# Performance work log

Hardware: AMD Instinct MI355X
Metric: run time of the kernel (lower is better)

The kernel has to match this reference:

```python
import jax, jax.numpy as jnp
import numpy as np

N_HEAD = 16
D_MODEL = 1024
D_K = D_MODEL // N_HEAD  # 64, also d_v
B, S = 8, 1024


def setup_inputs() -> dict:
    key = jax.random.key(0)
    ks = jax.random.split(key, 7)
    sc = 1.0 / np.sqrt(D_MODEL)
    return {
        "q": jax.random.normal(ks[0], (B, S, D_MODEL), jnp.float32),
        "k": jax.random.normal(ks[1], (B, S, D_MODEL), jnp.float32),
        "v": jax.random.normal(ks[2], (B, S, D_MODEL), jnp.float32),
        "Wq": jax.random.normal(ks[3], (N_HEAD, D_MODEL, D_K), jnp.float32) * sc,
        "Wk": jax.random.normal(ks[4], (N_HEAD, D_MODEL, D_K), jnp.float32) * sc,
        "Wv": jax.random.normal(ks[5], (D_MODEL, D_K), jnp.float32) * sc,  # shared across heads
        "Wo": jax.random.normal(ks[6], (D_K, D_MODEL), jnp.float32) * (1.0 / np.sqrt(D_K)),
    }


def reference(q, k, v, Wq, Wk, Wv, Wo):
    # Faithful to original: qs, ks, vs are ALL projected from q (k, v args unused),
    # and Wv is shared across all heads. Dropout is identity (rate 0 / eval).
    qs = jnp.einsum('bsd,hdk->hbsk', q, Wq)          # [H,B,S,dk]
    kk = jnp.einsum('bsd,hdk->hbsk', q, Wk)          # [H,B,S,dk]
    vs = jnp.einsum('bsd,dk->bsk', q, Wv)            # [B,S,dv] shared
    scale = 1.0 / jnp.sqrt(jnp.asarray(D_K, jnp.float32))
    scores = jnp.einsum('hbik,hbjk->hbij', qs, kk) * scale  # [H,B,S,S]
    attn = jax.nn.softmax(scores, axis=-1)
    head = jnp.einsum('hbij,bjk->hbik', attn, vs)    # [H,B,S,dv]
    pooled = jnp.mean(head, axis=0)                  # mean over heads, not concat
    out = jnp.einsum('bsk,kd->bsd', pooled, Wo)      # [B,S,d_model]
    return (out, attn)
```

## Files before the change

kernel.cpp:

```cpp
#include <hip/hip_runtime.h>
#include <hip/hip_bf16.h>
#include <stdint.h>

#define NC 2112

typedef __attribute__((ext_vector_type(8))) short bf16x8;
typedef __attribute__((ext_vector_type(4))) float f32x4;

static __device__ __forceinline__ unsigned short f2bf(float f) {
  uint32_t u = __builtin_bit_cast(uint32_t, f);
  u += 0x7FFFu + ((u >> 16) & 1u);
  return (unsigned short)(u >> 16);
}
static __device__ __forceinline__ float bf2f(unsigned short u) {
  return __builtin_bit_cast(float, ((uint32_t)u) << 16);
}
static __device__ __forceinline__ void gload16(const unsigned short* g, unsigned short* l) {
  __builtin_amdgcn_global_load_lds((const __attribute__((address_space(1))) void*)g,
                                   (__attribute__((address_space(3))) void*)l, 16, 0, 0);
}

__global__ void k_convert_q(const float* __restrict__ q, unsigned short* __restrict__ qbf) {
  int i = blockIdx.x * blockDim.x + threadIdx.x;
  float4 v = ((const float4*)q)[i];
  ushort4 o;
  o.x = f2bf(v.x); o.y = f2bf(v.y); o.z = f2bf(v.z); o.w = f2bf(v.w);
  ((ushort4*)qbf)[i] = o;
}

__global__ void k_build_wcatT(const float* __restrict__ Wq, const float* __restrict__ Wk,
                              const float* __restrict__ Wv, unsigned short* __restrict__ wt) {
  int t = blockIdx.x * blockDim.x + threadIdx.x;
  int c = t >> 7;
  int k0 = (t & 127) << 3;
  unsigned short o[8];
#pragma unroll
  for (int i = 0; i < 8; ++i) {
    int k = k0 + i;
    float v;
    if (c < 1024)      v = Wq[((size_t)(c >> 6) * 1024 + k) * 64 + (c & 63)];
    else if (c < 2048) v = Wk[((size_t)((c - 1024) >> 6) * 1024 + k) * 64 + (c & 63)];
    else               v = Wv[(size_t)k * 64 + (c - 2048)];
    o[i] = f2bf(v);
  }
  *(ushort4*)&wt[(size_t)c * 1024 + k0]     = *(ushort4*)&o[0];
  *(ushort4*)&wt[(size_t)c * 1024 + k0 + 4] = *(ushort4*)&o[4];
}

__global__ __launch_bounds__(256) void k_gemm(const unsigned short* __restrict__ A,
                                              const unsigned short* __restrict__ Bt,
                                              unsigned short* __restrict__ C,
                                              unsigned short* __restrict__ vst) {
  __shared__ unsigned short As[128 * 32];
  __shared__ unsigned short Bs[128 * 32];
  const int L = blockIdx.x;
  const int wi = (L & 7) * 136 + (L >> 3);
  const int tn = wi % 17, tm = wi / 17;
  const int rowBase = tm * 128, colBase = tn * 128;
  const int t = threadIdx.x;
  const int wave = t >> 6, lane = t & 63;
  const int wm = wave >> 1, wn = wave & 1;
  const int l15 = lane & 15, l4 = lane >> 4;
  f32x4 acc[4][4] = {};
  for (int kt = 0; kt < 1024; kt += 32) {
#pragma unroll
    for (int i = 0; i < 2; ++i) {
      int e = (t + i * 256) * 8;
      int r = e >> 5, c = e & 31;
      gload16(&A[(size_t)(rowBase + r) * 1024 + kt + c], &As[e]);
      int rb = colBase + r; rb = rb < NC ? rb : (NC - 1);
      gload16(&Bt[(size_t)rb * 1024 + kt + c], &Bs[e]);
    }
    __syncthreads();
    bf16x8 af[4], bfr[4];
#pragma unroll
    for (int m = 0; m < 4; ++m) af[m] = *(const bf16x8*)&As[(wm * 64 + m * 16 + l15) * 32 + l4 * 8];
#pragma unroll
    for (int n = 0; n < 4; ++n) bfr[n] = *(const bf16x8*)&Bs[(wn * 64 + n * 16 + l15) * 32 + l4 * 8];
#pragma unroll
    for (int m = 0; m < 4; ++m)
#pragma unroll
      for (int n = 0; n < 4; ++n)
        acc[m][n] = __builtin_amdgcn_mfma_f32_16x16x32_bf16(af[m], bfr[n], acc[m][n], 0, 0, 0);
    __syncthreads();
  }
#pragma unroll
  for (int m = 0; m < 4; ++m)
#pragma unroll
    for (int n = 0; n < 4; ++n) {
      int col = colBase + wn * 64 + n * 16 + l15;
      int row0 = rowBase + wm * 64 + m * 16 + l4 * 4;
      if (col < 2048) {
#pragma unroll
        for (int i = 0; i < 4; ++i)
          C[(size_t)(row0 + i) * NC + col] = f2bf(acc[m][n][i]);
      } else if (col < NC) {
        int d = col - 2048;
#pragma unroll
        for (int i = 0; i < 4; ++i) {
          int rg = row0 + i;
          vst[((size_t)(rg >> 10) * 64 + d) * 1024 + (rg & 1023)] = f2bf(acc[m][n][i]);
        }
      }
    }
}

__global__ __launch_bounds__(512, 4) void k_attn(const unsigned short* __restrict__ G,
                                                 const unsigned short* __restrict__ vst,
                                                 float* __restrict__ attn,
                                                 float* __restrict__ head) {
  __shared__ unsigned short SP[32][1032];
  __shared__ float rs[32][8];
  const int L = blockIdx.x;
  const int wi = (L & 7) * 512 + (L >> 3);
  const int qt = wi & 31, b = (wi >> 5) & 7, h = wi >> 8;
  const int t = threadIdx.x, wave = t >> 6, lane = t & 63;
  const int l15 = lane & 15, l4 = lane >> 4;

  const unsigned short* Gb = G + (size_t)b * 1024 * NC;

  bf16x8 qf[2][2];
#pragma unroll
  for (int m = 0; m < 2; ++m)
#pragma unroll
    for (int ks = 0; ks < 2; ++ks)
      qf[m][ks] = *(const bf16x8*)&Gb[(size_t)(qt * 32 + m * 16 + l15) * NC + h * 64 + ks * 32 + l4 * 8];

  const float scale = 0.125f;
  float psum[2][4] = {};
#pragma unroll
  for (int half = 0; half < 2; ++half) {
    bf16x8 kf[4][2];
#pragma unroll
    for (int kt = 0; kt < 4; ++kt) {
      int k0 = wave * 128 + (half * 4 + kt) * 16;
#pragma unroll
      for (int ks = 0; ks < 2; ++ks)
        kf[kt][ks] = *(const bf16x8*)&Gb[(size_t)(k0 + l15) * NC + 1024 + h * 64 + ks * 32 + l4 * 8];
    }
#pragma unroll
    for (int kt = 0; kt < 4; ++kt) {
      int k0 = wave * 128 + (half * 4 + kt) * 16;
      f32x4 s0 = {}, s1 = {};
      s0 = __builtin_amdgcn_mfma_f32_16x16x32_bf16(qf[0][0], kf[kt][0], s0, 0, 0, 0);
      s0 = __builtin_amdgcn_mfma_f32_16x16x32_bf16(qf[0][1], kf[kt][1], s0, 0, 0, 0);
      s1 = __builtin_amdgcn_mfma_f32_16x16x32_bf16(qf[1][0], kf[kt][0], s1, 0, 0, 0);
      s1 = __builtin_amdgcn_mfma_f32_16x16x32_bf16(qf[1][1], kf[kt][1], s1, 0, 0, 0);
#pragma unroll
      for (int i = 0; i < 4; ++i) {
        unsigned short u0 = f2bf(__expf(s0[i] * scale));
        unsigned short u1 = f2bf(__expf(s1[i] * scale));
        SP[l4 * 4 + i][k0 + l15]      = u0;
        SP[16 + l4 * 4 + i][k0 + l15] = u1;
        psum[0][i] += bf2f(u0);
        psum[1][i] += bf2f(u1);
      }
    }
  }
#pragma unroll
  for (int off = 1; off < 16; off <<= 1)
#pragma unroll
    for (int m = 0; m < 2; ++m)
#pragma unroll
      for (int i = 0; i < 4; ++i)
        psum[m][i] += __shfl_xor(psum[m][i], off);
  if (l15 == 0) {
#pragma unroll
    for (int m = 0; m < 2; ++m)
#pragma unroll
      for (int i = 0; i < 4; ++i)
        rs[m * 16 + l4 * 4 + i][wave] = psum[m][i];
  }
  __syncthreads();

  const int wm = wave >> 2, wn = wave & 3;
  float winv[4], pinv[4];
#pragma unroll
  for (int rr = 0; rr < 4; ++rr) {
    int row = wave * 4 + rr;
    float4 a = *(const float4*)&rs[row][0];
    float4 c = *(const float4*)&rs[row][4];
    winv[rr] = 1.0f / (a.x + a.y + a.z + a.w + c.x + c.y + c.z + c.w);
  }
#pragma unroll
  for (int i = 0; i < 4; ++i) {
    int row = wm * 16 + l4 * 4 + i;
    float4 a = *(const float4*)&rs[row][0];
    float4 c = *(const float4*)&rs[row][4];
    pinv[i] = 1.0f / (a.x + a.y + a.z + a.w + c.x + c.y + c.z + c.w);
  }

  size_t attn_base = ((size_t)(h * 8 + b) * 1024 + (size_t)qt * 32) * 1024;
#pragma unroll
  for (int rr = 0; rr < 4; ++rr) {
    int row = wave * 4 + rr;
    float inv = winv[rr];
#pragma unroll
    for (int c = 0; c < 2; ++c) {
      uint4 u = *(const uint4*)&SP[row][c * 512 + lane * 8];
      f32x4 p0 = {bf2f((unsigned short)(u.x & 0xFFFF)) * inv,
                  bf2f((unsigned short)(u.x >> 16)) * inv,
                  bf2f((unsigned short)(u.y & 0xFFFF)) * inv,
                  bf2f((unsigned short)(u.y >> 16)) * inv};
      f32x4 p1 = {bf2f((unsigned short)(u.z & 0xFFFF)) * inv,
                  bf2f((unsigned short)(u.z >> 16)) * inv,
                  bf2f((unsigned short)(u.w & 0xFFFF)) * inv,
                  bf2f((unsigned short)(u.w >> 16)) * inv};
      float* ab = &attn[attn_base + (size_t)row * 1024 + c * 512 + lane * 8];
      __builtin_nontemporal_store(p0, (f32x4*)ab);
      __builtin_nontemporal_store(p1, (f32x4*)(ab + 4));
    }
  }

  const unsigned short* vb = vst + ((size_t)b * 64 + wn * 16 + l15) * 1024;
  const unsigned short* pr = &SP[wm * 16 + l15][0];
  f32x4 o0 = {}, o1 = {};
#pragma unroll 8
  for (int jt = 0; jt < 32; jt += 2) {
    bf16x8 pa0 = *(const bf16x8*)&pr[jt * 32 + l4 * 8];
    bf16x8 bv0 = *(const bf16x8*)&vb[jt * 32 + l4 * 8];
    o0 = __builtin_amdgcn_mfma_f32_16x16x32_bf16(pa0, bv0, o0, 0, 0, 0);
    bf16x8 pa1 = *(const bf16x8*)&pr[(jt + 1) * 32 + l4 * 8];
    bf16x8 bv1 = *(const bf16x8*)&vb[(jt + 1) * 32 + l4 * 8];
    o1 = __builtin_amdgcn_mfma_f32_16x16x32_bf16(pa1, bv1, o1, 0, 0, 0);
  }
  float* hb = head + (((size_t)(h * 8 + b) * 1024) + qt * 32 + wm * 16) * 64 + wn * 16;
#pragma unroll
  for (int i = 0; i < 4; ++i)
    hb[(size_t)(l4 * 4 + i) * 64 + l15] = (o0[i] + o1[i]) * pinv[i];
}

__global__ __launch_bounds__(256) void k_final(const float* __restrict__ head,
                                               const float* __restrict__ Wo,
                                               float* __restrict__ out) {
  __shared__ float Ps[32][68];
  __shared__ float Ws[64][132];
  const int rt = blockIdx.x;
  const int r0 = rt * 32;
  const int t = threadIdx.x;
#pragma unroll
  for (int j = 0; j < 2; ++j) {
    int e = t + j * 256;
    int r = e >> 4, k4 = (e & 15) * 4;
    float4 acc = {0.f, 0.f, 0.f, 0.f};
#pragma unroll
    for (int hh = 0; hh < 16; ++hh) {
      float4 v = *(const float4*)&head[((size_t)hh * 8192 + r0 + r) * 64 + k4];
      acc.x += v.x; acc.y += v.y; acc.z += v.z; acc.w += v.w;
    }
    const float s = 1.0f / 16.0f;
    Ps[r][k4] = acc.x * s; Ps[r][k4 + 1] = acc.y * s;
    Ps[r][k4 + 2] = acc.z * s; Ps[r][k4 + 3] = acc.w * s;
  }
  const int ty = t >> 4, tx = t & 15;
  for (int dt = 0; dt < 8; ++dt) {
    int d0 = dt * 128;
#pragma unroll
    for (int j = 0; j < 8; ++j) {
      int e = t + j * 256;
      int k = e >> 5, c4 = (e & 31) * 4;
      *(float4*)&Ws[k][c4] = *(const float4*)&Wo[(size_t)k * 1024 + d0 + c4];
    }
    __syncthreads();
    float acc[2][8] = {};
    for (int k = 0; k < 64; ++k) {
      float a0 = Ps[ty * 2][k], a1 = Ps[ty * 2 + 1][k];
      float4 b0 = *(const float4*)&Ws[k][tx * 8];
      float4 b1 = *(const float4*)&Ws[k][tx * 8 + 4];
      acc[0][0] += a0 * b0.x; acc[0][1] += a0 * b0.y; acc[0][2] += a0 * b0.z; acc[0][3] += a0 * b0.w;
      acc[0][4] += a0 * b1.x; acc[0][5] += a0 * b1.y; acc[0][6] += a0 * b1.z; acc[0][7] += a0 * b1.w;
      acc[1][0] += a1 * b0.x; acc[1][1] += a1 * b0.y; acc[1][2] += a1 * b0.z; acc[1][3] += a1 * b0.w;
      acc[1][4] += a1 * b1.x; acc[1][5] += a1 * b1.y; acc[1][6] += a1 * b1.z; acc[1][7] += a1 * b1.w;
    }
#pragma unroll
    for (int i = 0; i < 2; ++i) {
      float4 v0 = {acc[i][0], acc[i][1], acc[i][2], acc[i][3]};
      float4 v1 = {acc[i][4], acc[i][5], acc[i][6], acc[i][7]};
      size_t o = (size_t)(r0 + ty * 2 + i) * 1024 + d0 + tx * 8;
      *(float4*)&out[o]     = v0;
      *(float4*)&out[o + 4] = v1;
    }
    __syncthreads();
  }
}

extern "C" void kernel_launch(void* const* d_in, const int* in_sizes, int n_in,
                              void* d_out, int out_size, void* d_ws, size_t ws_size,
                              hipStream_t stream) {
  const float* q  = (const float*)d_in[0];
  const float* Wq = (const float*)d_in[3];
  const float* Wk = (const float*)d_in[4];
  const float* Wv = (const float*)d_in[5];
  const float* Wo = (const float*)d_in[6];

  char* ws = (char*)d_ws;
  unsigned short* qbf   = (unsigned short*)(ws + 0);
  unsigned short* wcatT = (unsigned short*)(ws + 16777216);
  unsigned short* G     = (unsigned short*)(ws + 21102592);
  unsigned short* vst   = (unsigned short*)(ws + 55705600);
  float*          head  = (float*)(ws + 56754176);

  float* out  = (float*)d_out;
  float* attn = out + (size_t)8 * 1024 * 1024;

  hipLaunchKernelGGL(k_convert_q,   dim3(8192), dim3(256), 0, stream, q, qbf);
  hipLaunchKernelGGL(k_build_wcatT, dim3(1056), dim3(256), 0, stream, Wq, Wk, Wv, wcatT);
  hipLaunchKernelGGL(k_gemm,        dim3(1088), dim3(256), 0, stream, qbf, wcatT, G, vst);
  hipLaunchKernelGGL(k_attn,        dim3(4096), dim3(512), 0, stream, G, vst, attn, head);
  hipLaunchKernelGGL(k_final,       dim3(256),  dim3(256), 0, stream, head, Wo, out);
}
```

Measured before the change: 354.9 us.

## Shrink attention tile to 16 query rows with 4-wave blocks, halve final tile

The attention kernel now processes 16 query rows per block with 4 waves (256 threads) instead of 32 rows with 8 waves, doubling the grid. Each wave covers 256 keys, and the PV stage maps each wave to one 16-column slice of the head dimension. The final projection kernel halves its row tile to 16 and launches twice as many blocks. The manual bf16 rounding is swapped for the library __float2bfloat16 conversion. Smaller tiles cut LDS use per block and raise block count, but each K tile is now loaded per 16 query rows instead of 32, so K traffic per query row doubles.

```diff
diff --git a/kernel.cpp b/kernel.cpp
--- a/kernel.cpp
+++ b/kernel.cpp
@@ -11,6 +11,10 @@
   uint32_t u = __builtin_bit_cast(uint32_t, f);
   u += 0x7FFFu + ((u >> 16) & 1u);
   return (unsigned short)(u >> 16);
+}
+static __device__ __forceinline__ unsigned short f2bf_n(float f) {
+  __hip_bfloat16 h = __float2bfloat16(f);
+  return __builtin_bit_cast(unsigned short, h);
 }
 static __device__ __forceinline__ float bf2f(unsigned short u) {
   return __builtin_bit_cast(float, ((uint32_t)u) << 16);
@@ -93,104 +97,88 @@
       if (col < 2048) {
 #pragma unroll
         for (int i = 0; i < 4; ++i)
-          C[(size_t)(row0 + i) * NC + col] = f2bf(acc[m][n][i]);
+          C[(size_t)(row0 + i) * NC + col] = f2bf_n(acc[m][n][i]);
       } else if (col < NC) {
         int d = col - 2048;
 #pragma unroll
         for (int i = 0; i < 4; ++i) {
           int rg = row0 + i;
-          vst[((size_t)(rg >> 10) * 64 + d) * 1024 + (rg & 1023)] = f2bf(acc[m][n][i]);
+          vst[((size_t)(rg >> 10) * 64 + d) * 1024 + (rg & 1023)] = f2bf_n(acc[m][n][i]);
         }
       }
     }
 }
 
-__global__ __launch_bounds__(512, 4) void k_attn(const unsigned short* __restrict__ G,
+__global__ __launch_bounds__(256, 4) void k_attn(const unsigned short* __restrict__ G,
                                                  const unsigned short* __restrict__ vst,
                                                  float* __restrict__ attn,
                                                  float* __restrict__ head) {
-  __shared__ unsigned short SP[32][1032];
-  __shared__ float rs[32][8];
+  __shared__ unsigned short SP[16][1032];
+  __shared__ float rs[16][4];
   const int L = blockIdx.x;
-  const int wi = (L & 7) * 512 + (L >> 3);
-  const int qt = wi & 31, b = (wi >> 5) & 7, h = wi >> 8;
+  const int wi = (L & 7) * 1024 + (L >> 3);
+  const int qt = wi & 63, b = (wi >> 6) & 7, h = wi >> 9;
   const int t = threadIdx.x, wave = t >> 6, lane = t & 63;
   const int l15 = lane & 15, l4 = lane >> 4;
 
   const unsigned short* Gb = G + (size_t)b * 1024 * NC;
 
-  bf16x8 qf[2][2];
-#pragma unroll
-  for (int m = 0; m < 2; ++m)
-#pragma unroll
-    for (int ks = 0; ks < 2; ++ks)
-      qf[m][ks] = *(const bf16x8*)&Gb[(size_t)(qt * 32 + m * 16 + l15) * NC + h * 64 + ks * 32 + l4 * 8];
+  bf16x8 qf[2];
+#pragma unroll
+  for (int ks = 0; ks < 2; ++ks)
+    qf[ks] = *(const bf16x8*)&Gb[(size_t)(qt * 16 + l15) * NC + h * 64 + ks * 32 + l4 * 8];
 
   const float scale = 0.125f;
-  float psum[2][4] = {};
-#pragma unroll
-  for (int half = 0; half < 2; ++half) {
+  float psum[4] = {};
+#pragma unroll
+  for (int quarter = 0; quarter < 4; ++quarter) {
     bf16x8 kf[4][2];
 #pragma unroll
     for (int kt = 0; kt < 4; ++kt) {
-      int k0 = wave * 128 + (half * 4 + kt) * 16;
+      int k0 = wave * 256 + quarter * 64 + kt * 16;
 #pragma unroll
       for (int ks = 0; ks < 2; ++ks)
         kf[kt][ks] = *(const bf16x8*)&Gb[(size_t)(k0 + l15) * NC + 1024 + h * 64 + ks * 32 + l4 * 8];
     }
 #pragma unroll
     for (int kt = 0; kt < 4; ++kt) {
-      int k0 = wave * 128 + (half * 4 + kt) * 16;
-      f32x4 s0 = {}, s1 = {};
-      s0 = __builtin_amdgcn_mfma_f32_16x16x32_bf16(qf[0][0], kf[kt][0], s0, 0, 0, 0);
-      s0 = __builtin_amdgcn_mfma_f32_16x16x32_bf16(qf[0][1], kf[kt][1], s0, 0, 0, 0);
-      s1 = __builtin_amdgcn_mfma_f32_16x16x32_bf16(qf[1][0], kf[kt][0], s1, 0, 0, 0);
-      s1 = __builtin_amdgcn_mfma_f32_16x16x32_bf16(qf[1][1], kf[kt][1], s1, 0, 0, 0);
+      int k0 = wave * 256 + quarter * 64 + kt * 16;
+      f32x4 s0 = {};
+      s0 = __builtin_amdgcn_mfma_f32_16x16x32_bf16(qf[0], kf[kt][0], s0, 0, 0, 0);
+      s0 = __builtin_amdgcn_mfma_f32_16x16x32_bf16(qf[1], kf[kt][1], s0, 0, 0, 0);
 #pragma unroll
       for (int i = 0; i < 4; ++i) {
-        unsigned short u0 = f2bf(__expf(s0[i] * scale));
-        unsigned short u1 = f2bf(__expf(s1[i] * scale));
-        SP[l4 * 4 + i][k0 + l15]      = u0;
-        SP[16 + l4 * 4 + i][k0 + l15] = u1;
-        psum[0][i] += bf2f(u0);
-        psum[1][i] += bf2f(u1);
+        unsigned short u = f2bf_n(__expf(s0[i] * scale));
+        SP[l4 * 4 + i][k0 + l15] = u;
+        psum[i] += bf2f(u);
       }
     }
   }
 #pragma unroll
   for (int off = 1; off < 16; off <<= 1)
 #pragma unroll
-    for (int m = 0; m < 2; ++m)
-#pragma unroll
-      for (int i = 0; i < 4; ++i)
-        psum[m][i] += __shfl_xor(psum[m][i], off);
+    for (int i = 0; i < 4; ++i)
+      psum[i] += __shfl_xor(psum[i], off);
   if (l15 == 0) {
 #pragma unroll
-    for (int m = 0; m < 2; ++m)
-#pragma unroll
-      for (int i = 0; i < 4; ++i)
-        rs[m * 16 + l4 * 4 + i][wave] = psum[m][i];
+    for (int i = 0; i < 4; ++i)
+      rs[l4 * 4 + i][wave] = psum[i];
   }
   __syncthreads();
 
-  const int wm = wave >> 2, wn = wave & 3;
   float winv[4], pinv[4];
 #pragma unroll
   for (int rr = 0; rr < 4; ++rr) {
-    int row = wave * 4 + rr;
-    float4 a = *(const float4*)&rs[row][0];
-    float4 c = *(const float4*)&rs[row][4];
-    winv[rr] = 1.0f / (a.x + a.y + a.z + a.w + c.x + c.y + c.z + c.w);
+    float4 a = *(const float4*)&rs[wave * 4 + rr][0];
+    winv[rr] = 1.0f / (a.x + a.y + a.z + a.w);
   }
 #pragma unroll
   for (int i = 0; i < 4; ++i) {
-    int row = wm * 16 + l4 * 4 + i;
-    float4 a = *(const float4*)&rs[row][0];
-    float4 c = *(const float4*)&rs[row][4];
-    pinv[i] = 1.0f / (a.x + a.y + a.z + a.w + c.x + c.y + c.z + c.w);
-  }
-
-  size_t attn_base = ((size_t)(h * 8 + b) * 1024 + (size_t)qt * 32) * 1024;
+    float4 a = *(const float4*)&rs[l4 * 4 + i][0];
+    pinv[i] = 1.0f / (a.x + a.y + a.z + a.w);
+  }
+
+  size_t attn_base = ((size_t)(h * 8 + b) * 1024 + (size_t)qt * 16) * 1024;
 #pragma unroll
   for (int rr = 0; rr < 4; ++rr) {
     int row = wave * 4 + rr;
@@ -212,8 +200,8 @@
     }
   }
 
-  const unsigned short* vb = vst + ((size_t)b * 64 + wn * 16 + l15) * 1024;
-  const unsigned short* pr = &SP[wm * 16 + l15][0];
+  const unsigned short* vb = vst + ((size_t)b * 64 + wave * 16 + l15) * 1024;
+  const unsigned short* pr = &SP[l15][0];
   f32x4 o0 = {}, o1 = {};
 #pragma unroll 8
   for (int jt = 0; jt < 32; jt += 2) {
@@ -224,7 +212,7 @@
     bf16x8 bv1 = *(const bf16x8*)&vb[(jt + 1) * 32 + l4 * 8];
     o1 = __builtin_amdgcn_mfma_f32_16x16x32_bf16(pa1, bv1, o1, 0, 0, 0);
   }
-  float* hb = head + (((size_t)(h * 8 + b) * 1024) + qt * 32 + wm * 16) * 64 + wn * 16;
+  float* hb = head + (((size_t)(h * 8 + b) * 1024) + qt * 16) * 64 + wave * 16;
 #pragma unroll
   for (int i = 0; i < 4; ++i)
     hb[(size_t)(l4 * 4 + i) * 64 + l15] = (o0[i] + o1[i]) * pinv[i];
@@ -233,15 +221,13 @@
 __global__ __launch_bounds__(256) void k_final(const float* __restrict__ head,
                                                const float* __restrict__ Wo,
                                                float* __restrict__ out) {
-  __shared__ float Ps[32][68];
+  __shared__ float Ps[16][68];
   __shared__ float Ws[64][132];
   const int rt = blockIdx.x;
-  const int r0 = rt * 32;
+  const int r0 = rt * 16;
   const int t = threadIdx.x;
-#pragma unroll
-  for (int j = 0; j < 2; ++j) {
-    int e = t + j * 256;
-    int r = e >> 4, k4 = (e & 15) * 4;
+  {
+    int r = t >> 4, k4 = (t & 15) * 4;
     float4 acc = {0.f, 0.f, 0.f, 0.f};
 #pragma unroll
     for (int hh = 0; hh < 16; ++hh) {
@@ -262,24 +248,19 @@
       *(float4*)&Ws[k][c4] = *(const float4*)&Wo[(size_t)k * 1024 + d0 + c4];
     }
     __syncthreads();
-    float acc[2][8] = {};
+    float acc[8] = {};
     for (int k = 0; k < 64; ++k) {
-      float a0 = Ps[ty * 2][k], a1 = Ps[ty * 2 + 1][k];
+      float a0 = Ps[ty][k];
       float4 b0 = *(const float4*)&Ws[k][tx * 8];
       float4 b1 = *(const float4*)&Ws[k][tx * 8 + 4];
-      acc[0][0] += a0 * b0.x; acc[0][1] += a0 * b0.y; acc[0][2] += a0 * b0.z; acc[0][3] += a0 * b0.w;
-      acc[0][4] += a0 * b1.x; acc[0][5] += a0 * b1.y; acc[0][6] += a0 * b1.z; acc[0][7] += a0 * b1.w;
-      acc[1][0] += a1 * b0.x; acc[1][1] += a1 * b0.y; acc[1][2] += a1 * b0.z; acc[1][3] += a1 * b0.w;
-      acc[1][4] += a1 * b1.x; acc[1][5] += a1 * b1.y; acc[1][6] += a1 * b1.z; acc[1][7] += a1 * b1.w;
-    }
-#pragma unroll
-    for (int i = 0; i < 2; ++i) {
-      float4 v0 = {acc[i][0], acc[i][1], acc[i][2], acc[i][3]};
-      float4 v1 = {acc[i][4], acc[i][5], acc[i][6], acc[i][7]};
-      size_t o = (size_t)(r0 + ty * 2 + i) * 1024 + d0 + tx * 8;
-      *(float4*)&out[o]     = v0;
-      *(float4*)&out[o + 4] = v1;
-    }
+      acc[0] += a0 * b0.x; acc[1] += a0 * b0.y; acc[2] += a0 * b0.z; acc[3] += a0 * b0.w;
+      acc[4] += a0 * b1.x; acc[5] += a0 * b1.y; acc[6] += a0 * b1.z; acc[7] += a0 * b1.w;
+    }
+    float4 v0 = {acc[0], acc[1], acc[2], acc[3]};
+    float4 v1 = {acc[4], acc[5], acc[6], acc[7]};
+    size_t o = (size_t)(r0 + ty) * 1024 + d0 + tx * 8;
+    *(float4*)&out[o]     = v0;
+    *(float4*)&out[o + 4] = v1;
     __syncthreads();
   }
 }
@@ -306,6 +287,6 @@
   hipLaunchKernelGGL(k_convert_q,   dim3(8192), dim3(256), 0, stream, q, qbf);
   hipLaunchKernelGGL(k_build_wcatT, dim3(1056), dim3(256), 0, stream, Wq, Wk, Wv, wcatT);
   hipLaunchKernelGGL(k_gemm,        dim3(1088), dim3(256), 0, stream, qbf, wcatT, G, vst);
-  hipLaunchKernelGGL(k_attn,        dim3(4096), dim3(512), 0, stream, G, vst, attn, head);
-  hipLaunchKernelGGL(k_final,       dim3(256),  dim3(256), 0, stream, head, Wo, out);
-}
+  hipLaunchKernelGGL(k_attn,        dim3(8192), dim3(256), 0, stream, G, vst, attn, head);
+  hipLaunchKernelGGL(k_final,       dim3(512),  dim3(256), 0, stream, head, Wo, out);
+}
```

After: 401.5 us. 1.13x slower.
